# Optimization experiments

Measured on AMD Instinct MI355X. Metric: run time of the kernel, lower is better.

Reference implementation:

```python
import jax, jax.numpy as jnp
import numpy as np

BITS = 4
GROUP_SIZE = 128
IN_FEATURES = 4096
OUT_FEATURES = 14336
M = 256  # rows of x; >= kernel_switch_threshold so torch takes the dequant+matmul path


def setup_inputs() -> dict:
    key = jax.random.key(0)
    k1, k2, k3, k4 = jax.random.split(key, 4)
    x = jax.random.normal(k1, (M, IN_FEATURES), dtype=jnp.float16)
    # packed int4 weights: in_features//32*bits rows of int32
    qweight = jax.random.randint(
        k2, (IN_FEATURES // 32 * BITS, OUT_FEATURES), 0, 2**31 - 1, dtype=jnp.int32
    )
    n_groups = IN_FEATURES // GROUP_SIZE
    scales = jax.random.uniform(k3, (n_groups, OUT_FEATURES), dtype=jnp.float32) * 0.01 + 0.001
    # note: module stores zeros as scale*zero product (see pack()); any float works
    zeros = jax.random.uniform(k4, (n_groups, OUT_FEATURES), dtype=jnp.float32) * 0.05
    return {"x": x, "qweight": qweight, "scales": scales, "zeros": zeros}


def reference(x, qweight, scales, zeros):
    # Unpack 8 int4 values from each int32 (little-endian nibbles), matching
    # torch: (qweight[:,None,:] >> wf) & 0xF with wf = [0,4,...,28].
    shifts = jnp.arange(0, 32, BITS, dtype=jnp.int32)          # [8]
    w = (qweight[:, None, :] >> shifts[None, :, None]) & (2**BITS - 1)  # [K/8, 8, N]
    w = w.reshape(-1, GROUP_SIZE, qweight.shape[1])             # [n_groups, group, N]
    s = scales.astype(jnp.float16)[:, None, :]                  # [n_groups, 1, N]
    z = zeros.astype(jnp.float16)[:, None, :]
    # group-wise asymmetric dequant: scale * q - (scale*zero)
    w = (s * w.astype(jnp.float16) - z).reshape(-1, qweight.shape[1])  # [K, N]
    out = jnp.matmul(x, w)                                      # [M, N] fp16
    return out.astype(x.dtype)
```

## Files before the change

### kernel.cpp

```cpp
#include <hip/hip_runtime.h>

typedef unsigned int u32;
typedef unsigned short u16;
typedef __attribute__((ext_vector_type(8))) __bf16 bf16x8;
typedef __attribute__((ext_vector_type(4))) float f32x4;
typedef __attribute__((ext_vector_type(4))) u32 u32x4;

#define K_DIM 4096
#define N_DIM 14336
#define BM 128
#define BN 64
#define BK 64
#define NT (K_DIM / BK)
#define NBLK 448
#define LDA 72
#define LDB 72

__device__ __forceinline__ u32 pack_trunc(float lo, float hi) {
  return __builtin_amdgcn_perm(__float_as_uint(hi), __float_as_uint(lo), 0x07060302u);
}

__global__ __launch_bounds__(256, 2) void kivi_gemm(
    const float* __restrict__ X,
    const int* __restrict__ QW,
    const float* __restrict__ S,
    const float* __restrict__ Z,
    float* __restrict__ O)
{
  __shared__ __align__(16) u16 As[2][BM][LDA];
  __shared__ __align__(16) u16 Bs[2][BN][LDB];

  const int tid  = threadIdx.x;
  const int lane = tid & 63;
  const int w    = tid >> 6;

  const int b  = blockIdx.x;
  const int L  = (b & 7) * 56 + (b >> 3);
  const int m0 = (L & 1) * BM;
  const int n0 = (L >> 1) * BN;

  const int ncol  = tid & 63;
  const int k8r0  = tid >> 6;
  const int nglob = n0 + ncol;

  const int wm = w >> 1, wn = w & 1;
  const int mb = wm * 64, nb = wn * 32;
  const int fr = lane & 15, fq = lane >> 4;

  f32x4 acc[4][2];
#pragma unroll
  for (int mi = 0; mi < 4; ++mi)
#pragma unroll
    for (int ni = 0; ni < 2; ++ni)
      acc[mi][ni] = (f32x4){0.f, 0.f, 0.f, 0.f};

  u32x4 aPk[4];
  int qa, qb;
  float sv, zv;

  auto loadA = [&](int t) {
#pragma unroll
    for (int p = 0; p < 4; ++p) {
      const int ci  = p * 256 + tid;
      const int row = ci >> 3;
      const int c   = ci & 7;
      const float* src = X + (size_t)(m0 + row) * K_DIM + t * BK + c * 8;
      const f32x4 lo = *(const f32x4*)(src);
      const f32x4 hi = *(const f32x4*)(src + 4);
      aPk[p].x = pack_trunc(lo.x, lo.y);
      aPk[p].y = pack_trunc(lo.z, lo.w);
      aPk[p].z = pack_trunc(hi.x, hi.y);
      aPk[p].w = pack_trunc(hi.z, hi.w);
    }
  };
  auto writeA = [&](int buf) {
#pragma unroll
    for (int p = 0; p < 4; ++p) {
      const int ci  = p * 256 + tid;
      const int row = ci >> 3;
      const int c   = ci & 7;
      *(u32x4*)&As[buf][row][c * 8] = aPk[p];
    }
  };
  auto loadB = [&](int t) {
    const int r0 = t * 8 + k8r0;
    qa = QW[(size_t)r0 * N_DIM + nglob];
    qb = QW[(size_t)(r0 + 4) * N_DIM + nglob];
    sv = S[(size_t)(t >> 1) * N_DIM + nglob];
    zv = Z[(size_t)(t >> 1) * N_DIM + nglob];
  };
  auto writeB = [&](int buf) {
    const float cc = fmaf(-128.f, sv, -zv);
#pragma unroll
    for (int h = 0; h < 2; ++h) {
      const int q  = h ? qb : qa;
      const int k8 = k8r0 + h * 4;
      float wv[8];
#pragma unroll
      for (int j = 0; j < 8; ++j) {
        const u32 fb = 0x43000000u | (((u32)(q >> (4 * j)) & 0xFu) << 16);
        wv[j] = fmaf(sv, __uint_as_float(fb), cc);
      }
      u32x4 pk;
      pk.x = pack_trunc(wv[0], wv[1]);
      pk.y = pack_trunc(wv[2], wv[3]);
      pk.z = pack_trunc(wv[4], wv[5]);
      pk.w = pack_trunc(wv[6], wv[7]);
      *(u32x4*)&Bs[buf][ncol][k8 * 8] = pk;
    }
  };

  loadA(0); loadB(0);
  writeA(0); writeB(0);
  __syncthreads();

  for (int t = 0; t < NT; ++t) {
    const int cur = t & 1;
    const bool pf = (t + 1 < NT);
    if (pf) { loadA(t + 1); loadB(t + 1); }

#pragma unroll
    for (int ks = 0; ks < 2; ++ks) {
      bf16x8 af[4], bv[2];
#pragma unroll
      for (int mi = 0; mi < 4; ++mi)
        af[mi] = *(const bf16x8*)&As[cur][mb + mi * 16 + fr][ks * 32 + fq * 8];
#pragma unroll
      for (int ni = 0; ni < 2; ++ni)
        bv[ni] = *(const bf16x8*)&Bs[cur][nb + ni * 16 + fr][ks * 32 + fq * 8];
#pragma unroll
      for (int mi = 0; mi < 4; ++mi)
#pragma unroll
        for (int ni = 0; ni < 2; ++ni)
          acc[mi][ni] = __builtin_amdgcn_mfma_f32_16x16x32_bf16(
              af[mi], bv[ni], acc[mi][ni], 0, 0, 0);
    }

    if (pf) { writeA(cur ^ 1); writeB(cur ^ 1); }
    __syncthreads();
  }

#pragma unroll
  for (int mi = 0; mi < 4; ++mi)
#pragma unroll
    for (int ni = 0; ni < 2; ++ni)
#pragma unroll
      for (int r = 0; r < 4; ++r) {
        const int row = m0 + mb + mi * 16 + fq * 4 + r;
        const int col = n0 + nb + ni * 16 + fr;
        O[(size_t)row * N_DIM + col] = acc[mi][ni][r];
      }
}

extern "C" void kernel_launch(void* const* d_in, const int* in_sizes, int n_in,
                              void* d_out, int out_size, void* d_ws, size_t ws_size,
                              hipStream_t stream) {
  const float* X  = (const float*)d_in[0];
  const int*   QW = (const int*)d_in[1];
  const float* S  = (const float*)d_in[2];
  const float* Zp = (const float*)d_in[3];
  float* O = (float*)d_out;
  hipLaunchKernelGGL(kivi_gemm, dim3(NBLK), dim3(256), 0, stream, X, QW, S, Zp, O);
}
```

Before: 77.68 us.

## Split K across two warp-groups, switch to fp16 MFMA with packed half2 dequant

```diff
diff --git a/kernel.cpp b/kernel.cpp
--- a/kernel.cpp
+++ b/kernel.cpp
@@ -1,8 +1,9 @@
 #include <hip/hip_runtime.h>
+#include <hip/hip_fp16.h>
 
 typedef unsigned int u32;
 typedef unsigned short u16;
-typedef __attribute__((ext_vector_type(8))) __bf16 bf16x8;
+typedef __attribute__((ext_vector_type(8))) _Float16 f16x8;
 typedef __attribute__((ext_vector_type(4))) float f32x4;
 typedef __attribute__((ext_vector_type(4))) u32 u32x4;
 
@@ -11,16 +12,24 @@
 #define BM 128
 #define BN 64
 #define BK 64
-#define NT (K_DIM / BK)
+#define NT 64
 #define NBLK 448
 #define LDA 72
 #define LDB 72
 
-__device__ __forceinline__ u32 pack_trunc(float lo, float hi) {
-  return __builtin_amdgcn_perm(__float_as_uint(hi), __float_as_uint(lo), 0x07060302u);
+union H2U { u32 u; __half2 h; };
+
+__device__ __forceinline__ u32 pkrtz(float a, float b) {
+  return __builtin_bit_cast(u32, __builtin_amdgcn_cvt_pkrtz(a, b));
 }
 
-__global__ __launch_bounds__(256, 2) void kivi_gemm(
+__device__ __forceinline__ u32 dq2(u32 t, __half2 s2, __half2 c2) {
+  H2U x; x.u = 0x58005800u | ((t & 0xFu) << 3) | ((t & 0xF0u) << 15);
+  H2U r; r.h = __hfma2(s2, x.h, c2);
+  return r.u;
+}
+
+__global__ __launch_bounds__(512, 4) void kivi_gemm(
     const float* __restrict__ X,
     const int* __restrict__ QW,
     const float* __restrict__ S,
@@ -33,17 +42,20 @@
   const int tid  = threadIdx.x;
   const int lane = tid & 63;
   const int w    = tid >> 6;
+  const int ws   = w >> 2;
+  const int wl   = w & 3;
+  const int stid = tid & 255;
 
   const int b  = blockIdx.x;
   const int L  = (b & 7) * 56 + (b >> 3);
   const int m0 = (L & 1) * BM;
   const int n0 = (L >> 1) * BN;
 
-  const int ncol  = tid & 63;
-  const int k8r0  = tid >> 6;
+  const int ncol  = stid & 63;
+  const int k8r0  = stid >> 6;
   const int nglob = n0 + ncol;
 
-  const int wm = w >> 1, wn = w & 1;
+  const int wm = wl >> 1, wn = wl & 1;
   const int mb = wm * 64, nb = wn * 32;
   const int fr = lane & 15, fq = lane >> 4;
 
@@ -61,25 +73,25 @@
   auto loadA = [&](int t) {
 #pragma unroll
     for (int p = 0; p < 4; ++p) {
-      const int ci  = p * 256 + tid;
+      const int ci  = p * 256 + stid;
       const int row = ci >> 3;
       const int c   = ci & 7;
       const float* src = X + (size_t)(m0 + row) * K_DIM + t * BK + c * 8;
       const f32x4 lo = *(const f32x4*)(src);
       const f32x4 hi = *(const f32x4*)(src + 4);
-      aPk[p].x = pack_trunc(lo.x, lo.y);
-      aPk[p].y = pack_trunc(lo.z, lo.w);
-      aPk[p].z = pack_trunc(hi.x, hi.y);
-      aPk[p].w = pack_trunc(hi.z, hi.w);
+      aPk[p].x = pkrtz(lo.x, lo.y);
+      aPk[p].y = pkrtz(lo.z, lo.w);
+      aPk[p].z = pkrtz(hi.x, hi.y);
+      aPk[p].w = pkrtz(hi.z, hi.w);
     }
   };
-  auto writeA = [&](int buf) {
+  auto writeA = [&]() {
 #pragma unroll
     for (int p = 0; p < 4; ++p) {
-      const int ci  = p * 256 + tid;
+      const int ci  = p * 256 + stid;
       const int row = ci >> 3;
       const int c   = ci & 7;
-      *(u32x4*)&As[buf][row][c * 8] = aPk[p];
+      *(u32x4*)&As[ws][row][c * 8] = aPk[p];
     }
   };
   auto loadB = [&](int t) {
@@ -89,67 +101,77 @@
     sv = S[(size_t)(t >> 1) * N_DIM + nglob];
     zv = Z[(size_t)(t >> 1) * N_DIM + nglob];
   };
-  auto writeB = [&](int buf) {
-    const float cc = fmaf(-128.f, sv, -zv);
+  auto writeB = [&]() {
+    const __half sh = __float2half(sv);
+    const __half ch = __float2half(fmaf(-128.f, sv, -zv));
+    const __half2 s2 = __halves2half2(sh, sh);
+    const __half2 c2 = __halves2half2(ch, ch);
 #pragma unroll
     for (int h = 0; h < 2; ++h) {
-      const int q  = h ? qb : qa;
+      const u32 q  = (u32)(h ? qb : qa);
       const int k8 = k8r0 + h * 4;
-      float wv[8];
-#pragma unroll
-      for (int j = 0; j < 8; ++j) {
-        const u32 fb = 0x43000000u | (((u32)(q >> (4 * j)) & 0xFu) << 16);
-        wv[j] = fmaf(sv, __uint_as_float(fb), cc);
-      }
       u32x4 pk;
-      pk.x = pack_trunc(wv[0], wv[1]);
-      pk.y = pack_trunc(wv[2], wv[3]);
-      pk.z = pack_trunc(wv[4], wv[5]);
-      pk.w = pack_trunc(wv[6], wv[7]);
-      *(u32x4*)&Bs[buf][ncol][k8 * 8] = pk;
+      pk.x = dq2(q,       s2, c2);
+      pk.y = dq2(q >> 8,  s2, c2);
+      pk.z = dq2(q >> 16, s2, c2);
+      pk.w = dq2(q >> 24, s2, c2);
+      *(u32x4*)&Bs[ws][ncol][k8 * 8] = pk;
     }
   };
 
-  loadA(0); loadB(0);
-  writeA(0); writeB(0);
+  loadA(ws); loadB(ws);
+  writeA(); writeB();
   __syncthreads();
 
-  for (int t = 0; t < NT; ++t) {
-    const int cur = t & 1;
-    const bool pf = (t + 1 < NT);
-    if (pf) { loadA(t + 1); loadB(t + 1); }
+  for (int i = 0; i < NT / 2; ++i) {
+    const bool pf = (i + 1 < NT / 2);
+    if (pf) { loadA(2 * i + 2 + ws); loadB(2 * i + 2 + ws); }
 
 #pragma unroll
     for (int ks = 0; ks < 2; ++ks) {
-      bf16x8 af[4], bv[2];
+      f16x8 af[4], bv[2];
 #pragma unroll
       for (int mi = 0; mi < 4; ++mi)
-        af[mi] = *(const bf16x8*)&As[cur][mb + mi * 16 + fr][ks * 32 + fq * 8];
+        af[mi] = *(const f16x8*)&As[ws][mb + mi * 16 + fr][ks * 32 + fq * 8];
 #pragma unroll
       for (int ni = 0; ni < 2; ++ni)
-        bv[ni] = *(const bf16x8*)&Bs[cur][nb + ni * 16 + fr][ks * 32 + fq * 8];
+        bv[ni] = *(const f16x8*)&Bs[ws][nb + ni * 16 + fr][ks * 32 + fq * 8];
 #pragma unroll
       for (int mi = 0; mi < 4; ++mi)
 #pragma unroll
         for (int ni = 0; ni < 2; ++ni)
-          acc[mi][ni] = __builtin_amdgcn_mfma_f32_16x16x32_bf16(
+          acc[mi][ni] = __builtin_amdgcn_mfma_f32_16x16x32_f16(
               af[mi], bv[ni], acc[mi][ni], 0, 0, 0);
     }
 
-    if (pf) { writeA(cur ^ 1); writeB(cur ^ 1); }
+    __syncthreads();
+    if (pf) { writeA(); writeB(); }
     __syncthreads();
   }
 
+  float (*Lr)[68] = reinterpret_cast<float(*)[68]>(&As[0][0][0]);
+  if (ws == 1) {
 #pragma unroll
-  for (int mi = 0; mi < 4; ++mi)
+    for (int mi = 0; mi < 4; ++mi)
 #pragma unroll
-    for (int ni = 0; ni < 2; ++ni)
+      for (int ni = 0; ni < 2; ++ni)
 #pragma unroll
-      for (int r = 0; r < 4; ++r) {
-        const int row = m0 + mb + mi * 16 + fq * 4 + r;
-        const int col = n0 + nb + ni * 16 + fr;
-        O[(size_t)row * N_DIM + col] = acc[mi][ni][r];
-      }
+        for (int r = 0; r < 4; ++r)
+          Lr[mb + mi * 16 + fq * 4 + r][nb + ni * 16 + fr] = acc[mi][ni][r];
+  }
+  __syncthreads();
+  if (ws == 0) {
+#pragma unroll
+    for (int mi = 0; mi < 4; ++mi)
+#pragma unroll
+      for (int ni = 0; ni < 2; ++ni)
+#pragma unroll
+        for (int r = 0; r < 4; ++r) {
+          const int row = mb + mi * 16 + fq * 4 + r;
+          const int col = nb + ni * 16 + fr;
+          O[(size_t)(m0 + row) * N_DIM + n0 + col] = acc[mi][ni][r] + Lr[row][col];
+        }
+  }
 }
 
 extern "C" void kernel_launch(void* const* d_in, const int* in_sizes, int n_in,
@@ -160,5 +182,5 @@
   const float* S  = (const float*)d_in[2];
   const float* Zp = (const float*)d_in[3];
   float* O = (float*)d_out;
-  hipLaunchKernelGGL(kivi_gemm, dim3(NBLK), dim3(256), 0, stream, X, QW, S, Zp, O);
+  hipLaunchKernelGGL(kivi_gemm, dim3(NBLK), dim3(512), 0, stream, X, QW, S, Zp, O);
 }
```

Result: faster. 65.31 us (-15.9%).

## Split-K in two halves with atomics, wider N tile, fp16 dequant via magic-number trick

Applied to the files above, without the earlier changes.

```diff
diff --git a/kernel.cpp b/kernel.cpp
--- a/kernel.cpp
+++ b/kernel.cpp
@@ -1,23 +1,46 @@
 #include <hip/hip_runtime.h>
+#include <hip/hip_fp16.h>
 
 typedef unsigned int u32;
 typedef unsigned short u16;
-typedef __attribute__((ext_vector_type(8))) __bf16 bf16x8;
+typedef __attribute__((ext_vector_type(8))) _Float16 f16x8;
 typedef __attribute__((ext_vector_type(4))) float f32x4;
 typedef __attribute__((ext_vector_type(4))) u32 u32x4;
 
+#define M_DIM 256
 #define K_DIM 4096
 #define N_DIM 14336
 #define BM 128
-#define BN 64
+#define BN 128
 #define BK 64
-#define NT (K_DIM / BK)
+#define KHALF (K_DIM / 2)
+#define NITER (KHALF / BK)
 #define NBLK 448
 #define LDA 72
-#define LDB 72
 
-__device__ __forceinline__ u32 pack_trunc(float lo, float hi) {
-  return __builtin_amdgcn_perm(__float_as_uint(hi), __float_as_uint(lo), 0x07060302u);
+union U4F8 { u32x4 u; f16x8 v; };
+
+__device__ __forceinline__ f16x8 dq8(u32 q, __half2 s2, __half2 d2, __half2 z2) {
+  const u32 q1 = q >> 4, q2 = q >> 8, q3 = q >> 12;
+  U4F8 r;
+  const u32 x0 = ( q & 0x000F000Fu) | 0x64006400u;
+  const u32 x1 = (q1 & 0x000F000Fu) | 0x64006400u;
+  const u32 x2 = (q2 & 0x000F000Fu) | 0x64006400u;
+  const u32 x3 = (q3 & 0x000F000Fu) | 0x64006400u;
+  r.u.x = __builtin_bit_cast(u32, __hsub2(__hfma2(__builtin_bit_cast(__half2, x0), s2, d2), z2));
+  r.u.y = __builtin_bit_cast(u32, __hsub2(__hfma2(__builtin_bit_cast(__half2, x1), s2, d2), z2));
+  r.u.z = __builtin_bit_cast(u32, __hsub2(__hfma2(__builtin_bit_cast(__half2, x2), s2, d2), z2));
+  r.u.w = __builtin_bit_cast(u32, __hsub2(__hfma2(__builtin_bit_cast(__half2, x3), s2, d2), z2));
+  return r.v;
+}
+
+__device__ __forceinline__ u32 pkrtz(float a, float b) {
+  return __builtin_bit_cast(u32, __builtin_amdgcn_cvt_pkrtz(a, b));
+}
+
+__global__ void zero_out(float* __restrict__ O) {
+  const size_t i = (size_t)blockIdx.x * 256 + threadIdx.x;
+  ((f32x4*)O)[i] = (f32x4){0.f, 0.f, 0.f, 0.f};
 }
 
 __global__ __launch_bounds__(256, 2) void kivi_gemm(
@@ -28,85 +51,80 @@
     float* __restrict__ O)
 {
   __shared__ __align__(16) u16 As[2][BM][LDA];
-  __shared__ __align__(16) u16 Bs[2][BN][LDB];
+  __shared__ __align__(16) u16 Bs[2][BN][LDA];
 
   const int tid  = threadIdx.x;
   const int lane = tid & 63;
   const int w    = tid >> 6;
 
-  const int b  = blockIdx.x;
-  const int L  = (b & 7) * 56 + (b >> 3);
-  const int m0 = (L & 1) * BM;
-  const int n0 = (L >> 1) * BN;
-
-  const int ncol  = tid & 63;
-  const int k8r0  = tid >> 6;
-  const int nglob = n0 + ncol;
+  const int b   = blockIdx.x;
+  const int L   = (b & 7) * 56 + (b >> 3);
+  const int kh  = L / 224;
+  const int rem = L % 224;
+  const int mt  = rem / 112;
+  const int nt  = rem % 112;
+  const int m0  = mt * BM;
+  const int n0  = nt * BN;
+  const int kb  = kh * KHALF;
+  const int kb8 = kh * (KHALF / 8);
 
   const int wm = w >> 1, wn = w & 1;
-  const int mb = wm * 64, nb = wn * 32;
+  const int mb = wm * 64, nb = wn * 64;
   const int fr = lane & 15, fq = lane >> 4;
 
-  f32x4 acc[4][2];
+  const int arow = tid >> 1;
+  const int aseg = tid & 1;
+  const int bcol  = tid >> 1;
+  const int bhalf = tid & 1;
+  const int colg  = n0 + bcol;
+
+  f32x4 acc[4][4];
 #pragma unroll
   for (int mi = 0; mi < 4; ++mi)
 #pragma unroll
-    for (int ni = 0; ni < 2; ++ni)
+    for (int ni = 0; ni < 4; ++ni)
       acc[mi][ni] = (f32x4){0.f, 0.f, 0.f, 0.f};
 
-  u32x4 aPk[4];
-  int qa, qb;
+  f32x4 aR[8];
+  u32 qR[4];
   float sv, zv;
 
   auto loadA = [&](int t) {
+    const float* p = X + (size_t)(m0 + arow) * K_DIM + kb + t * BK + aseg * 32;
 #pragma unroll
-    for (int p = 0; p < 4; ++p) {
-      const int ci  = p * 256 + tid;
-      const int row = ci >> 3;
-      const int c   = ci & 7;
-      const float* src = X + (size_t)(m0 + row) * K_DIM + t * BK + c * 8;
-      const f32x4 lo = *(const f32x4*)(src);
-      const f32x4 hi = *(const f32x4*)(src + 4);
-      aPk[p].x = pack_trunc(lo.x, lo.y);
-      aPk[p].y = pack_trunc(lo.z, lo.w);
-      aPk[p].z = pack_trunc(hi.x, hi.y);
-      aPk[p].w = pack_trunc(hi.z, hi.w);
-    }
+    for (int c = 0; c < 8; ++c) aR[c] = *(const f32x4*)(p + c * 4);
   };
   auto writeA = [&](int buf) {
 #pragma unroll
-    for (int p = 0; p < 4; ++p) {
-      const int ci  = p * 256 + tid;
-      const int row = ci >> 3;
-      const int c   = ci & 7;
-      *(u32x4*)&As[buf][row][c * 8] = aPk[p];
+    for (int c = 0; c < 4; ++c) {
+      u32x4 pk;
+      pk.x = pkrtz(aR[c * 2][0], aR[c * 2 + 1][0]);
+      pk.y = pkrtz(aR[c * 2][1], aR[c * 2 + 1][1]);
+      pk.z = pkrtz(aR[c * 2][2], aR[c * 2 + 1][2]);
+      pk.w = pkrtz(aR[c * 2][3], aR[c * 2 + 1][3]);
+      *(u32x4*)&As[buf][arow][aseg * 32 + c * 8] = pk;
     }
   };
   auto loadB = [&](int t) {
-    const int r0 = t * 8 + k8r0;
-    qa = QW[(size_t)r0 * N_DIM + nglob];
-    qb = QW[(size_t)(r0 + 4) * N_DIM + nglob];
-    sv = S[(size_t)(t >> 1) * N_DIM + nglob];
-    zv = Z[(size_t)(t >> 1) * N_DIM + nglob];
+    const size_t rbase = (size_t)(kb8 + t * 8 + bhalf * 4) * N_DIM + colg;
+#pragma unroll
+    for (int j = 0; j < 4; ++j)
+      qR[j] = *(const u32*)(QW + rbase + (size_t)j * N_DIM);
+    const int g = kh * 16 + (t >> 1);
+    sv = S[(size_t)g * N_DIM + colg];
+    zv = Z[(size_t)g * N_DIM + colg];
   };
   auto writeB = [&](int buf) {
-    const float cc = fmaf(-128.f, sv, -zv);
+    const __half sh = __float2half(sv);
+    const __half zh = __float2half(zv);
+    const __half dh = __hmul(sh, __float2half(-1024.f));
+    const __half2 s2 = __halves2half2(sh, sh);
+    const __half2 d2 = __halves2half2(dh, dh);
+    const __half2 z2 = __halves2half2(zh, zh);
 #pragma unroll
-    for (int h = 0; h < 2; ++h) {
-      const int q  = h ? qb : qa;
-      const int k8 = k8r0 + h * 4;
-      float wv[8];
-#pragma unroll
-      for (int j = 0; j < 8; ++j) {
-        const u32 fb = 0x43000000u | (((u32)(q >> (4 * j)) & 0xFu) << 16);
-        wv[j] = fmaf(sv, __uint_as_float(fb), cc);
-      }
-      u32x4 pk;
-      pk.x = pack_trunc(wv[0], wv[1]);
-      pk.y = pack_trunc(wv[2], wv[3]);
-      pk.z = pack_trunc(wv[4], wv[5]);
-      pk.w = pack_trunc(wv[6], wv[7]);
-      *(u32x4*)&Bs[buf][ncol][k8 * 8] = pk;
+    for (int j = 0; j < 4; ++j) {
+      const f16x8 v = dq8(qR[j], s2, d2, z2);
+      *(f16x8*)&Bs[buf][bcol][(bhalf * 4 + j) * 8] = v;
     }
   };
 
@@ -114,26 +132,27 @@
   writeA(0); writeB(0);
   __syncthreads();
 
-  for (int t = 0; t < NT; ++t) {
+#pragma unroll 1
+  for (int t = 0; t < NITER; ++t) {
     const int cur = t & 1;
-    const bool pf = (t + 1 < NT);
+    const bool pf = (t + 1 < NITER);
     if (pf) { loadA(t + 1); loadB(t + 1); }
 
 #pragma unroll
     for (int ks = 0; ks < 2; ++ks) {
-      bf16x8 af[4], bv[2];
+      f16x8 af[4], bf[4];
 #pragma unroll
       for (int mi = 0; mi < 4; ++mi)
-        af[mi] = *(const bf16x8*)&As[cur][mb + mi * 16 + fr][ks * 32 + fq * 8];
+        af[mi] = *(const f16x8*)&As[cur][mb + mi * 16 + fr][ks * 32 + fq * 8];
 #pragma unroll
-      for (int ni = 0; ni < 2; ++ni)
-        bv[ni] = *(const bf16x8*)&Bs[cur][nb + ni * 16 + fr][ks * 32 + fq * 8];
+      for (int ni = 0; ni < 4; ++ni)
+        bf[ni] = *(const f16x8*)&Bs[cur][nb + ni * 16 + fr][ks * 32 + fq * 8];
 #pragma unroll
       for (int mi = 0; mi < 4; ++mi)
 #pragma unroll
-        for (int ni = 0; ni < 2; ++ni)
-          acc[mi][ni] = __builtin_amdgcn_mfma_f32_16x16x32_bf16(
-              af[mi], bv[ni], acc[mi][ni], 0, 0, 0);
+        for (int ni = 0; ni < 4; ++ni)
+          acc[mi][ni] = __builtin_amdgcn_mfma_f32_16x16x32_f16(
+              af[mi], bf[ni], acc[mi][ni], 0, 0, 0);
     }
 
     if (pf) { writeA(cur ^ 1); writeB(cur ^ 1); }
@@ -143,12 +162,12 @@
 #pragma unroll
   for (int mi = 0; mi < 4; ++mi)
 #pragma unroll
-    for (int ni = 0; ni < 2; ++ni)
+    for (int ni = 0; ni < 4; ++ni)
 #pragma unroll
       for (int r = 0; r < 4; ++r) {
         const int row = m0 + mb + mi * 16 + fq * 4 + r;
         const int col = n0 + nb + ni * 16 + fr;
-        O[(size_t)row * N_DIM + col] = acc[mi][ni][r];
+        atomicAdd(&O[(size_t)row * N_DIM + col], acc[mi][ni][r]);
       }
 }
 
@@ -160,5 +179,6 @@
   const float* S  = (const float*)d_in[2];
   const float* Zp = (const float*)d_in[3];
   float* O = (float*)d_out;
+  hipLaunchKernelGGL(zero_out, dim3(3584), dim3(256), 0, stream, O);
   hipLaunchKernelGGL(kivi_gemm, dim3(NBLK), dim3(256), 0, stream, X, QW, S, Zp, O);
 }
```

Measured after the change: 99.60 us. +28.2%, slower.
